# Kernel tuning notes

Measured on AMD Instinct MI355X. Metric: run time of the kernel, lower is better.

Reference implementation:

```python
import jax, jax.numpy as jnp
import numpy as np
from functools import partial

VOCAB = 1000
HID = 512
EPS = 1e-3  # Keras BatchNorm default epsilon


def _conv1d(x, w, stride):
    # x: [B,T,C_in], w: [K,C_in,C_out]
    return jax.lax.conv_general_dilated(x, w, window_strides=(stride,), padding='SAME',
                                        dimension_numbers=('NWC', 'WIO', 'NWC'))


def setup_inputs() -> dict:
    key = jax.random.key(0)
    ks = jax.random.split(key, 8)
    s = lambda *sh: 1.0 / np.sqrt(sh[-2] if len(sh) > 1 else sh[-1])
    return {
        'x': jax.random.normal(ks[0], (32, 1600, 80), jnp.float32),
        'y_true': jax.random.randint(ks[1], (32, 201), 0, VOCAB),
        'bn_gamma': jnp.ones((80,), jnp.float32),
        'bn_beta': jnp.zeros((80,), jnp.float32),
        'conv0_w': jax.random.normal(ks[2], (5, 80, 512), jnp.float32) * 0.05,
        'conv0_b': jnp.zeros((512,), jnp.float32),
        'tcr_w': jax.random.normal(ks[3], (4, 5, 512, 512), jnp.float32) * 0.02,
        'tcr_b': jnp.zeros((4, 512), jnp.float32),
        'gru_kernel': jax.random.normal(ks[4], (VOCAB, 3 * HID), jnp.float32) * 0.03,
        'gru_rec_kernel': jax.random.normal(ks[5], (HID, 3 * HID), jnp.float32) * 0.04,
        'gru_bias': jnp.zeros((2, 3 * HID), jnp.float32),
        'fc_w': jax.random.normal(ks[6], (2 * HID, VOCAB), jnp.float32) * 0.03,
        'fc_b': jnp.zeros((VOCAB,), jnp.float32),
    }


def reference(x, y_true, bn_gamma, bn_beta, conv0_w, conv0_b, tcr_w, tcr_b,
              gru_kernel, gru_rec_kernel, gru_bias, fc_w, fc_b):
    # ---- Encoder ----
    # BatchNorm (training mode: batch statistics over batch & time)
    mean = jnp.mean(x, axis=(0, 1))
    var = jnp.var(x, axis=(0, 1))
    h = (x - mean) * jax.lax.rsqrt(var + EPS) * bn_gamma + bn_beta
    # strided Conv1D + relu -> [B, T=800, 512]
    h = jax.nn.relu(_conv1d(h, conv0_w, 2) + conv0_b)
    # Temporal conv residual blocks: out = relu(conv(x)) + x
    for i in range(tcr_w.shape[0]):
        h = jax.nn.relu(_conv1d(h, tcr_w[i], 1) + tcr_b[i]) + h
    enc = h  # [B, T, D]
    B = enc.shape[0]

    # ---- Decoder (teacher forcing, training branch) ----
    y_oh = jax.nn.one_hot(y_true, VOCAB, dtype=jnp.float32)  # [B, U+1, V]
    inputs = jnp.transpose(y_oh[:, :-1, :], (1, 0, 2))       # [U, B, V]
    bi, br = gru_bias[0], gru_bias[1]

    def step(hstate, y_u):
        # Keras GRUCell (reset_after=True)
        mx = y_u @ gru_kernel + bi
        mh = hstate @ gru_rec_kernel + br
        xz, xr, xh = jnp.split(mx, 3, axis=-1)
        hz, hr, hh = jnp.split(mh, 3, axis=-1)
        z = jax.nn.sigmoid(xz + hz)
        r = jax.nn.sigmoid(xr + hr)
        cand = jnp.tanh(xh + r * hh)
        h_new = z * hstate + (1.0 - z) * cand
        # Dot-product attention over encoder states
        scores = jnp.einsum('bd,btd->bt', h_new, enc)
        alpha = jax.nn.softmax(scores, axis=-1)
        ctx = jnp.einsum('bt,btd->bd', alpha, enc)
        # output projection with softmax activation
        y_pred = jax.nn.softmax(jnp.concatenate([h_new, ctx], axis=1) @ fc_w + fc_b, axis=-1)
        return h_new, y_pred

    h0 = jnp.zeros((B, HID), jnp.float32)
    _, outs = jax.lax.scan(step, h0, inputs)  # [U, B, V]
    return jnp.transpose(outs, (1, 0, 2))     # [B, U, V]
```

## Files before the change

### kernel.cpp

```cpp
#include <hip/hip_runtime.h>
#include <cstdint>

typedef _Float16 f16;
typedef __attribute__((ext_vector_type(2))) _Float16 f16x2;
typedef __attribute__((ext_vector_type(8))) _Float16 f16x8;
typedef __attribute__((ext_vector_type(4))) float f32x4;
typedef __attribute__((ext_vector_type(2))) float f32x2;
typedef __attribute__((ext_vector_type(8))) unsigned short us8;
typedef __attribute__((ext_vector_type(4))) int i32x4;

#define NB   32
#define TIN  1600
#define CIN  80
#define TOUT 800
#define DH   512
#define NV   1000
#define NU   200
#define TXP  1604
#define THP  804
#define EPSB 1e-3f
#define EWG  248

__device__ __forceinline__ void st_sys_f16(f16* p, float v)
{
    f16 h = (f16)v;
    short s; __builtin_memcpy(&s, &h, 2);
    int si = (int)s;
    asm volatile("global_store_short %0, %1, off sc0 sc1"
                 :: "v"(p), "v"(si) : "memory");
}

__device__ __forceinline__ void poll_h16(const f16* base, f16x8 v[16])
{
    while (true) {
        asm volatile(
            "global_load_dwordx4 %0, %16, off sc1\n\t"
            "global_load_dwordx4 %1, %16, off offset:64 sc1\n\t"
            "global_load_dwordx4 %2, %16, off offset:128 sc1\n\t"
            "global_load_dwordx4 %3, %16, off offset:192 sc1\n\t"
            "global_load_dwordx4 %4, %16, off offset:256 sc1\n\t"
            "global_load_dwordx4 %5, %16, off offset:320 sc1\n\t"
            "global_load_dwordx4 %6, %16, off offset:384 sc1\n\t"
            "global_load_dwordx4 %7, %16, off offset:448 sc1\n\t"
            "global_load_dwordx4 %8, %16, off offset:512 sc1\n\t"
            "global_load_dwordx4 %9, %16, off offset:576 sc1\n\t"
            "global_load_dwordx4 %10, %16, off offset:640 sc1\n\t"
            "global_load_dwordx4 %11, %16, off offset:704 sc1\n\t"
            "global_load_dwordx4 %12, %16, off offset:768 sc1\n\t"
            "global_load_dwordx4 %13, %16, off offset:832 sc1\n\t"
            "global_load_dwordx4 %14, %16, off offset:896 sc1\n\t"
            "global_load_dwordx4 %15, %16, off offset:960 sc1\n\t"
            "s_waitcnt vmcnt(0)"
            : "=&v"(v[0]), "=&v"(v[1]), "=&v"(v[2]), "=&v"(v[3]),
              "=&v"(v[4]), "=&v"(v[5]), "=&v"(v[6]), "=&v"(v[7]),
              "=&v"(v[8]), "=&v"(v[9]), "=&v"(v[10]), "=&v"(v[11]),
              "=&v"(v[12]), "=&v"(v[13]), "=&v"(v[14]), "=&v"(v[15])
            : "v"(base)
            : "memory");
        f16x8 s0 = v[0] + v[1],   s1 = v[2] + v[3];
        f16x8 s2 = v[4] + v[5],   s3 = v[6] + v[7];
        f16x8 s4 = v[8] + v[9],   s5 = v[10] + v[11];
        f16x8 s6 = v[12] + v[13], s7 = v[14] + v[15];
        s0 += s1; s2 += s3; s4 += s5; s6 += s7;
        s0 += s2; s4 += s6; s0 += s4;
        float r = (float)s0[0] + (float)s0[1] + (float)s0[2] + (float)s0[3]
                + (float)s0[4] + (float)s0[5] + (float)s0[6] + (float)s0[7];
        if (!__any(r != r)) return;
        __builtin_amdgcn_s_sleep(1);
    }
}

__device__ __forceinline__ float fast_tanh(float x)
{
    return 1.f - 2.f / (__expf(2.f * x) + 1.f);
}

__global__ void init_zero(float* gsum, float* gsumsq,
                          int* lcnt, f16* xpad, f16* hbufA, f16* hbufB,
                          f16* Hc)
{
    int tid = blockIdx.x * 256 + threadIdx.x;
    int stride = gridDim.x * 256;
    if (blockIdx.x == 0) {
        if (threadIdx.x < 80) { gsum[threadIdx.x] = 0.f; gsumsq[threadIdx.x] = 0.f; }
        if (threadIdx.x >= 128 && threadIdx.x < 136) lcnt[threadIdx.x - 128] = 0;
    }
    for (int i = tid; i < NB * 4 * CIN; i += stride) {
        int b = i / (4 * CIN), rr = (i / CIN) % 4, c = i % CIN;
        int row = (rr == 0) ? 0 : (1600 + rr);
        xpad[((long)b * TXP + row) * CIN + c] = (f16)0.f;
    }
    for (int i = tid; i < 2 * NB * 4 * DH; i += stride) {
        int q = i; int buf = q / (NB * 4 * DH); q %= NB * 4 * DH;
        int b = q / (4 * DH); int rr = (q / DH) % 4; int dd = q % DH;
        int row = (rr < 2) ? rr : (800 + rr);
        f16* hb = buf ? hbufB : hbufA;
        hb[((long)b * THP + row) * DH + dd] = (f16)0.f;
    }
    us8 sent;
#pragma unroll
    for (int e = 0; e < 8; e++) sent[e] = 0x7FFFu;
    for (int i = tid; i < 6400 * 64; i += stride)
        *(us8*)&Hc[(long)(i >> 6) * 1024 + (i & 63) * 8] = sent;
}

__global__ void transpose_f32_f16(const float* __restrict__ in, int R, int C,
                                  f16* __restrict__ out, int outRows, int outCols)
{
    __shared__ float t[32][33];
    int c0 = blockIdx.x * 32, r0 = blockIdx.y * 32;
    int x = threadIdx.x & 31, y = threadIdx.x >> 5;
    for (int i = y; i < 32; i += 8) {
        int r = r0 + i, c = c0 + x;
        t[i][x] = (r < R && c < C) ? in[(long)r * C + c] : 0.0f;
    }
    __syncthreads();
    for (int i = y; i < 32; i += 8) {
        int orow = c0 + i, ocol = r0 + x;
        if (orow < outRows && ocol < outCols)
            out[(long)orow * outCols + ocol] = (f16)t[x][i];
    }
}

__global__ void bn_stats(const float* __restrict__ x, float* gsum, float* gsumsq)
{
    __shared__ float ls[240], ls2[240];
    const float* base = x + (long)blockIdx.x * 200 * CIN;
    int tid = threadIdx.x;
    if (tid < 240) {
        int c = tid % 80, rg = tid / 80;
        float s = 0.f, s2 = 0.f;
        for (int r = rg; r < 200; r += 3) {
            float v = base[r * CIN + c];
            s += v; s2 += v * v;
        }
        ls[tid] = s; ls2[tid] = s2;
    }
    __syncthreads();
    if (tid < 80) {
        atomicAdd(&gsum[tid],   ls[tid] + ls[tid + 80] + ls[tid + 160]);
        atomicAdd(&gsumsq[tid], ls2[tid] + ls2[tid + 80] + ls2[tid + 160]);
    }
}

__global__ void bn_apply(const float* __restrict__ x, const float* __restrict__ gsum,
                         const float* __restrict__ gsumsq, const float* __restrict__ gamma,
                         const float* __restrict__ beta, f16* __restrict__ xpad)
{
    long idx = (long)blockIdx.x * 256 + threadIdx.x;
    if (idx >= (long)NB * TIN * CIN) return;
    int c = (int)(idx % CIN);
    long bt = idx / CIN;
    int t = (int)(bt % TIN); int b = (int)(bt / TIN);
    float mean = gsum[c] * (1.f / 51200.f);
    float var  = gsumsq[c] * (1.f / 51200.f) - mean * mean;
    float sc = gamma[c] * rsqrtf(var + EPSB);
    float sh = beta[c] - mean * sc;
    xpad[((long)b * TXP + t + 1) * CIN + c] = (f16)(x[idx] * sc + sh);
}

template<int MODE>
__launch_bounds__(256)
__global__ void gemm16(const f16* __restrict__ Ab, long strideA, long slabA,
                       const f16* __restrict__ Bb, long strideB, long slabB,
                       int M, int N, int Kchunks,
                       const float* __restrict__ bias,
                       float* __restrict__ outF)
{
    __shared__ f16 As[64][72];
    __shared__ f16 Bs[128][72];
    const int b = blockIdx.z;
    const f16* Abase = Ab + (long)b * slabA;
    const f16* Bbase = Bb + (long)b * slabB;
    const int m0 = blockIdx.x * 64, n0 = blockIdx.y * 128;
    const int tid = threadIdx.x;
    const int lane = tid & 63, wv = tid >> 6;
    const int lm = lane & 15, lk = lane >> 4;

    f32x4 vzero = {0.f, 0.f, 0.f, 0.f};
    f32x4 acc[4][2];
#pragma unroll
    for (int i = 0; i < 4; i++) { acc[i][0] = vzero; acc[i][1] = vzero; }

    const int srow = tid >> 3, scol = (tid & 7) * 8;

    for (int kc = 0; kc < Kchunks; kc++) {
        int kb = kc * 64;
#pragma unroll
        for (int p = 0; p < 2; p++) {
            int r = srow + p * 32;
            int m = m0 + r; if (m > M - 1) m = M - 1;
            *(us8*)&As[r][scol] = *(const us8*)(Abase + (long)m * strideA + kb + scol);
        }
#pragma unroll
        for (int p = 0; p < 4; p++) {
            int r = srow + p * 32;
            int n = n0 + r; if (n > N - 1) n = N - 1;
            *(us8*)&Bs[r][scol] = *(const us8*)(Bbase + (long)n * strideB + kb + scol);
        }
        __syncthreads();
#pragma unroll
        for (int ks = 0; ks < 2; ks++) {
            f16x8 af[4], bf[2];
#pragma unroll
            for (int mt = 0; mt < 4; mt++)
                af[mt] = *(const f16x8*)&As[mt * 16 + lm][ks * 32 + lk * 8];
#pragma unroll
            for (int nt = 0; nt < 2; nt++)
                bf[nt] = *(const f16x8*)&Bs[wv * 32 + nt * 16 + lm][ks * 32 + lk * 8];
#pragma unroll
            for (int mt = 0; mt < 4; mt++)
#pragma unroll
                for (int nt = 0; nt < 2; nt++)
                    acc[mt][nt] = __builtin_amdgcn_mfma_f32_16x16x32_f16(af[mt], bf[nt], acc[mt][nt], 0, 0, 0);
        }
        __syncthreads();
    }
#pragma unroll
    for (int mt = 0; mt < 4; mt++) {
#pragma unroll
        for (int nt = 0; nt < 2; nt++) {
            int n = n0 + wv * 32 + nt * 16 + lm;
#pragma unroll
            for (int reg = 0; reg < 4; reg++) {
                int m = m0 + mt * 16 + lk * 4 + reg;
                if (m >= M || n >= N) continue;
                float v = acc[mt][nt][reg];
                if (MODE == 2) {
                    outF[((long)b * NU + m) * 800 + n] = v;
                } else {
                    v += bias[n];
                    int u = m >> 5, bb = m & 31;
                    outF[((long)bb * NU + u) * 1000 + n] = v;
                }
            }
        }
    }
}

__device__ void enc_layer(int eb, int tid,
                          const f16* __restrict__ Ab, long strideA, long slabA,
                          const f16* __restrict__ Bb, long strideB,
                          int Kchunks, const float* __restrict__ bias,
                          const f16* __restrict__ resid, f16* __restrict__ outH,
                          long slabRO, f16 As[][72], f16 Bs[][72])
{
    const int lane = tid & 63, wv = tid >> 6;
    const int lm = lane & 15, lk = lane >> 4;
    const int srow = tid >> 3, scol = (tid & 7) * 8;
    f32x4 vzero = {0.f, 0.f, 0.f, 0.f};

    for (int t = eb; t < 1664; t += EWG) {
        int b = t / 52, rem = t - b * 52;
        int m0 = (rem >> 2) * 64, n0 = (rem & 3) * 128;
        const f16* Abase = Ab + (long)b * slabA;

        f32x4 acc[4][2];
#pragma unroll
        for (int i = 0; i < 4; i++) { acc[i][0] = vzero; acc[i][1] = vzero; }

        for (int kc = 0; kc < Kchunks; kc++) {
            int kb = kc * 64;
#pragma unroll
            for (int p = 0; p < 2; p++) {
                int r = srow + p * 32;
                int m = m0 + r; if (m > 799) m = 799;
                *(us8*)&As[r][scol] = *(const us8*)(Abase + (long)m * strideA + kb + scol);
            }
#pragma unroll
            for (int p = 0; p < 4; p++) {
                int r = srow + p * 32;
                *(us8*)&Bs[r][scol] = *(const us8*)(Bb + (long)(n0 + r) * strideB + kb + scol);
            }
            __syncthreads();
#pragma unroll
            for (int ks = 0; ks < 2; ks++) {
                f16x8 af[4], bf[2];
#pragma unroll
                for (int mt = 0; mt < 4; mt++)
                    af[mt] = *(const f16x8*)&As[mt * 16 + lm][ks * 32 + lk * 8];
#pragma unroll
                for (int nt = 0; nt < 2; nt++)
                    bf[nt] = *(const f16x8*)&Bs[wv * 32 + nt * 16 + lm][ks * 32 + lk * 8];
#pragma unroll
                for (int mt = 0; mt < 4; mt++)
#pragma unroll
                    for (int nt = 0; nt < 2; nt++)
                        acc[mt][nt] = __builtin_amdgcn_mfma_f32_16x16x32_f16(af[mt], bf[nt], acc[mt][nt], 0, 0, 0);
            }
            __syncthreads();
        }
#pragma unroll
        for (int mt = 0; mt < 4; mt++) {
#pragma unroll
            for (int nt = 0; nt < 2; nt++) {
                int n = n0 + wv * 32 + nt * 16 + lm;
#pragma unroll
                for (int reg = 0; reg < 4; reg++) {
                    int m = m0 + mt * 16 + lk * 4 + reg;
                    if (m >= 800) continue;
                    float v = acc[mt][nt][reg] + bias[n];
                    v = v > 0.f ? v : 0.f;
                    if (resid) v += (float)resid[(long)b * slabRO + (long)(2 + m) * DH + n];
                    outH[(long)b * slabRO + (long)(2 + m) * DH + n] = (f16)v;
                }
            }
        }
    }
}

__launch_bounds__(256, 1)
__global__ void enc_gru(const f16* __restrict__ wrecT, const float* __restrict__ gk,
                        const float* __restrict__ gbias, const int* __restrict__ ytrue,
                        f16* __restrict__ Hc,
                        const f16* __restrict__ xpad, const f16* __restrict__ w0T,
                        const float* __restrict__ b0, const f16* __restrict__ tcrT,
                        const float* __restrict__ tcrb,
                        f16* __restrict__ hbufA, f16* __restrict__ hbufB,
                        int* __restrict__ lcnt)
{
    const int tid = threadIdx.x;

    if (blockIdx.x < 8) {
        __shared__ int yl[NU * 32];
        const int lane = tid & 63, wv = tid >> 6;
        const int gw = (int)blockIdx.x * 4 + wv;
        const int lm = lane & 15, lk = lane >> 4;
        const int j = gw * 16 + lm;

        for (int i = tid; i < NU * 32; i += 256) {
            int b = i / NU, u = i - b * NU;
            yl[u * 32 + b] = ytrue[b * 201 + u];
        }

        f16x8 wf[3][16];
#pragma unroll
        for (int g = 0; g < 3; g++)
#pragma unroll
            for (int ks = 0; ks < 16; ks++) {
                wf[g][ks] = *(const f16x8*)&wrecT[(long)(g * 512 + j) * 512 + ks * 32 + lk * 8];
                asm volatile("" : "+v"(wf[g][ks]));
            }

        const float biz = gbias[j],        bir = gbias[512 + j],        bic = gbias[1024 + j];
        const float brz = gbias[1536 + j], brr = gbias[1536 + 512 + j], brc = gbias[1536 + 1024 + j];
        f32x4 vzero = {0.f, 0.f, 0.f, 0.f};

        __syncthreads();

        float hold[8];
        float nxz[8], nxr[8], nxh[8], mxz[8], mxr[8], mxh[8];
#pragma unroll
        for (int s = 0; s < 8; s++) {
            hold[s] = 0.f;
            int b = ((s >> 2) << 4) + lk * 4 + (s & 3);
            const float* gkr = gk + (long)yl[b] * 1536;
            nxz[s] = gkr[j]; nxr[s] = gkr[512 + j]; nxh[s] = gkr[1024 + j];
        }

        for (int u = 0; u < NU; u++) {
            int up = (u < NU - 1) ? u + 1 : u;
#pragma unroll
            for (int s = 0; s < 8; s++) {
                int b = ((s >> 2) << 4) + lk * 4 + (s & 3);
                const float* gkr = gk + (long)yl[up * 32 + b] * 1536;
                mxz[s] = gkr[j]; mxr[s] = gkr[512 + j]; mxh[s] = gkr[1024 + j];
            }

            f32x4 acc[3][2];
#pragma unroll
            for (int g = 0; g < 3; g++) { acc[g][0] = vzero; acc[g][1] = vzero; }

            if (u > 0) {
                const f16* baseA = Hc + ((long)(u - 1) * 32 + lm) * 1024 + lk * 8;
                {
                    f16x8 va[16];
                    poll_h16(baseA, va);
#pragma unroll
                    for (int ks = 0; ks < 16; ks++)
#pragma unroll
                        for (int g = 0; g < 3; g++)
                            acc[g][0] = __builtin_amdgcn_mfma_f32_16x16x32_f16(va[ks], wf[g][ks], acc[g][0], 0, 0, 0);
                }
                {
                    f16x8 vb[16];
                    poll_h16(baseA + 16 * 1024, vb);
#pragma unroll
                    for (int ks = 0; ks < 16; ks++)
#pragma unroll
                        for (int g = 0; g < 3; g++)
                            acc[g][1] = __builtin_amdgcn_mfma_f32_16x16x32_f16(vb[ks], wf[g][ks], acc[g][1], 0, 0, 0);
                }
            }

#pragma unroll
            for (int mt = 0; mt < 2; mt++) {
#pragma unroll
                for (int reg = 0; reg < 4; reg++) {
                    int s = mt * 4 + reg;
                    int b = mt * 16 + lk * 4 + reg;
                    float hz = acc[0][mt][reg] + brz;
                    float hr = acc[1][mt][reg] + brr;
                    float hh = acc[2][mt][reg] + brc;
                    float z = 1.f / (1.f + __expf(-(nxz[s] + biz + hz)));
                    float r = 1.f / (1.f + __expf(-(nxr[s] + bir + hr)));
                    float cd = fast_tanh(nxh[s] + bic + r * hh);
                    float hnew = z * hold[s] + (1.f - z) * cd;
                    hold[s] = hnew;
                    st_sys_f16(&Hc[((long)u * 32 + b) * 1024 + j], hnew);
                }
            }
#pragma unroll
            for (int s = 0; s < 8; s++) { nxz[s] = mxz[s]; nxr[s] = mxr[s]; nxh[s] = mxh[s]; }
        }
        asm volatile("s_waitcnt vmcnt(0)" ::: "memory");
        return;
    }

    __shared__ f16 As[64][72];
    __shared__ f16 Bs[128][72];
    const int eb = (int)blockIdx.x - 8;

    enc_layer(eb, tid, xpad, 160, (long)TXP * CIN, w0T, 448, 7, b0,
              nullptr, hbufA, (long)THP * DH, As, Bs);

    const f16* tin = hbufA; f16* tout = hbufB;
    for (int L = 0; L < 4; L++) {
        __syncthreads();
        if (tid == 0) {
            __hip_atomic_fetch_add(&lcnt[L], 1, __ATOMIC_RELEASE, __HIP_MEMORY_SCOPE_AGENT);
            while (__hip_atomic_load(&lcnt[L], __ATOMIC_RELAXED, __HIP_MEMORY_SCOPE_AGENT) < EWG)
                __builtin_amdgcn_s_sleep(8);
            (void)__hip_atomic_load(&lcnt[L], __ATOMIC_ACQUIRE, __HIP_MEMORY_SCOPE_AGENT);
        }
        __syncthreads();

        enc_layer(eb, tid, tin, 512, (long)THP * DH, tcrT + (size_t)L * 512 * 2560, 2560,
                  40, tcrb + L * 512, tin, tout, (long)THP * DH, As, Bs);
        const f16* t2 = tout; tout = (f16*)tin; tin = t2;
    }
}

__global__ void row_softmax(float* __restrict__ base, int len)
{
    float* s = base + (long)blockIdx.x * len;
    int tid = threadIdx.x;
    float v[4]; float mx = -1e30f;
#pragma unroll
    for (int i = 0; i < 4; i++) {
        int idx = tid + i * 256;
        v[i] = (idx < len) ? s[idx] : -1e30f;
        mx = fmaxf(mx, v[i]);
    }
#pragma unroll
    for (int off = 32; off; off >>= 1) mx = fmaxf(mx, __shfl_xor(mx, off));
    __shared__ float red[4], red2[4];
    if ((tid & 63) == 0) red[tid >> 6] = mx;
    __syncthreads();
    mx = fmaxf(fmaxf(red[0], red[1]), fmaxf(red[2], red[3]));
    float sum = 0.f;
#pragma unroll
    for (int i = 0; i < 4; i++) { v[i] = __expf(v[i] - mx); sum += v[i]; }
#pragma unroll
    for (int off = 32; off; off >>= 1) sum += __shfl_xor(sum, off);
    if ((tid & 63) == 0) red2[tid >> 6] = sum;
    __syncthreads();
    sum = red2[0] + red2[1] + red2[2] + red2[3];
    float inv = 1.f / sum;
#pragma unroll
    for (int i = 0; i < 4; i++) {
        int idx = tid + i * 256;
        if (idx < len) s[idx] = v[i] * inv;
    }
}

__global__ void ctx_kernel(const float* __restrict__ scores, const f16* __restrict__ enc,
                           f16* __restrict__ Hc)
{
    __shared__ float al[800][18];
    __shared__ float red[4], red2[4];
    int b = blockIdx.x, ut = blockIdx.y;
    int u0 = ut * 16;
    int tid = threadIdx.x;
    for (int ul = 0; ul < 16; ul++) {
        int u = u0 + ul;
        if (u < NU) {
            const float* arow = scores + ((long)b * NU + u) * 800;
            float v[4]; float mx = -1e30f;
#pragma unroll
            for (int i = 0; i < 4; i++) {
                int idx = tid + i * 256;
                v[i] = (idx < 800) ? arow[idx] : -1e30f;
                mx = fmaxf(mx, v[i]);
            }
#pragma unroll
            for (int off = 32; off; off >>= 1) mx = fmaxf(mx, __shfl_xor(mx, off));
            if ((tid & 63) == 0) red[tid >> 6] = mx;
            __syncthreads();
            mx = fmaxf(fmaxf(red[0], red[1]), fmaxf(red[2], red[3]));
            float sum = 0.f;
#pragma unroll
            for (int i = 0; i < 4; i++) { v[i] = __expf(v[i] - mx); sum += v[i]; }
#pragma unroll
            for (int off = 32; off; off >>= 1) sum += __shfl_xor(sum, off);
            if ((tid & 63) == 0) red2[tid >> 6] = sum;
            __syncthreads();
            sum = red2[0] + red2[1] + red2[2] + red2[3];
            float inv = 1.f / sum;
#pragma unroll
            for (int i = 0; i < 4; i++) {
                int idx = tid + i * 256;
                if (idx < 800) al[idx][ul] = v[i] * inv;
            }
            __syncthreads();
        } else {
            for (int t = tid; t < 800; t += 256) al[t][ul] = 0.f;
        }
    }
    __syncthreads();
    int d0 = tid * 2;
    float a0[16], a1[16];
#pragma unroll
    for (int i = 0; i < 16; i++) { a0[i] = 0.f; a1[i] = 0.f; }
    const f16* encb = enc + ((long)b * THP + 2) * DH + d0;
    for (int t = 0; t < 800; t++) {
        f16x2 e = *(const f16x2*)&encb[(long)t * DH];
        float f0 = (float)e.x, f1 = (float)e.y;
#pragma unroll
        for (int g = 0; g < 8; g++) {
            f32x2 ap = *(const f32x2*)&al[t][2 * g];
            a0[2 * g]     += ap.x * f0; a0[2 * g + 1] += ap.y * f0;
            a1[2 * g]     += ap.x * f1; a1[2 * g + 1] += ap.y * f1;
        }
    }
#pragma unroll
    for (int ul = 0; ul < 16; ul++) {
        int u = u0 + ul;
        if (u < NU) {
            Hc[((long)u * 32 + b) * 1024 + 512 + d0]     = (f16)a0[ul];
            Hc[((long)u * 32 + b) * 1024 + 512 + d0 + 1] = (f16)a1[ul];
        }
    }
}

extern "C" void kernel_launch(void* const* d_in, const int* in_sizes, int n_in,
                              void* d_out, int out_size, void* d_ws, size_t ws_size,
                              hipStream_t stream)
{
    const float* x     = (const float*)d_in[0];
    const int*   ytrue = (const int*)d_in[1];
    const float* gamma = (const float*)d_in[2];
    const float* beta  = (const float*)d_in[3];
    const float* w0    = (const float*)d_in[4];
    const float* b0    = (const float*)d_in[5];
    const float* tcrw  = (const float*)d_in[6];
    const float* tcrb  = (const float*)d_in[7];
    const float* gk    = (const float*)d_in[8];
    const float* grk   = (const float*)d_in[9];
    const float* gbias = (const float*)d_in[10];
    const float* fcw   = (const float*)d_in[11];
    const float* fcb   = (const float*)d_in[12];
    float* out = (float*)d_out;
    (void)in_sizes; (void)n_in; (void)out_size; (void)ws_size;

    char* ws = (char*)d_ws;
    size_t o = 0;
    auto alloc = [&](size_t bytes) { size_t r = o; o += (bytes + 255) & ~(size_t)255; return r; };
    f16*   xpad   = (f16*)(ws + alloc((size_t)NB * TXP * CIN * 2));
    f16*   hbufA  = (f16*)(ws + alloc((size_t)NB * THP * DH * 2));
    f16*   hbufB  = (f16*)(ws + alloc((size_t)NB * THP * DH * 2));
    f16*   Hc     = (f16*)(ws + alloc((size_t)NU * NB * 1024 * 2));
    float* scores = (float*)(ws + alloc((size_t)NB * NU * 800 * 4));
    f16*   w0T    = (f16*)(ws + alloc((size_t)512 * 448 * 2));
    f16*   tcrT   = (f16*)(ws + alloc((size_t)4 * 512 * 2560 * 2));
    f16*   wrecT  = (f16*)(ws + alloc((size_t)1536 * 512 * 2));
    f16*   fcT    = (f16*)(ws + alloc((size_t)1024 * 1024 * 2));
    float* gsum   = (float*)(ws + alloc(80 * 4));
    float* gsumsq = (float*)(ws + alloc(80 * 4));
    int*   lcnt   = (int*)(ws + alloc(64));

    init_zero<<<64, 256, 0, stream>>>(gsum, gsumsq, lcnt, xpad, hbufA, hbufB, Hc);
    transpose_f32_f16<<<dim3(16, 14), 256, 0, stream>>>(w0, 400, 512, w0T, 512, 448);
    for (int i = 0; i < 4; i++)
        transpose_f32_f16<<<dim3(16, 80), 256, 0, stream>>>(tcrw + (size_t)i * 2560 * 512, 2560, 512,
                                                            tcrT + (size_t)i * 512 * 2560, 512, 2560);
    transpose_f32_f16<<<dim3(48, 16), 256, 0, stream>>>(grk, 512, 1536, wrecT, 1536, 512);
    transpose_f32_f16<<<dim3(32, 32), 256, 0, stream>>>(fcw, 1024, 1000, fcT, 1024, 1024);

    bn_stats<<<256, 256, 0, stream>>>(x, gsum, gsumsq);
    bn_apply<<<16000, 256, 0, stream>>>(x, gsum, gsumsq, gamma, beta, xpad);

    enc_gru<<<8 + EWG, 256, 0, stream>>>(wrecT, gk, gbias, ytrue, Hc,
                                         xpad, w0T, b0, tcrT, tcrb, hbufA, hbufB, lcnt);
    const f16* enc = hbufA;

    gemm16<2><<<dim3(4, 7, 32), 256, 0, stream>>>(Hc, 32 * 1024, 1024, enc + 2 * DH, 512, (long)THP * DH,
        200, 800, 8, nullptr, scores);
    ctx_kernel<<<dim3(32, 13), 256, 0, stream>>>(scores, enc, Hc);

    gemm16<3><<<dim3(100, 8, 1), 256, 0, stream>>>(Hc, 1024, 0, fcT, 1024, 0,
        6400, 1000, 16, fcb, out);
    row_softmax<<<6400, 256, 0, stream>>>(out, 1000);
}
```

Measured before the change: 1.653 ms.

## Fuse attention score GEMM into context kernel using MFMA into shared memory

Removes the separate score GEMM launch and its fp32 scores buffer. Each attention block now computes its own 16x800 score tile with 16x16x32 f16 MFMAs, writes it straight into shared memory, then runs the softmax and context accumulation as before. This saves a global round-trip of the scores and one launch. In exchange, the score work is spread across only 416 blocks, and the same Hc buffer is both read (the h half) and written (the ctx half) in one kernel.

```diff
diff --git a/kernel.cpp b/kernel.cpp
--- a/kernel.cpp
+++ b/kernel.cpp
@@ -474,23 +474,50 @@
     }
 }
 
-__global__ void ctx_kernel(const float* __restrict__ scores, const f16* __restrict__ enc,
-                           f16* __restrict__ Hc)
+__launch_bounds__(256)
+__global__ void attn_kernel(const f16* __restrict__ HcIn, const f16* __restrict__ enc,
+                            f16* __restrict__ Hc)
 {
     __shared__ float al[800][18];
     __shared__ float red[4], red2[4];
-    int b = blockIdx.x, ut = blockIdx.y;
-    int u0 = ut * 16;
-    int tid = threadIdx.x;
+    const int b = blockIdx.x, ut = blockIdx.y;
+    const int u0 = ut * 16;
+    const int tid = threadIdx.x;
+    const int lane = tid & 63, wv = tid >> 6;
+    const int lm = lane & 15, lk = lane >> 4;
+
+    int ua = u0 + lm; if (ua > NU - 1) ua = NU - 1;
+    const f16* arow = HcIn + ((long)ua * 32 + b) * 1024 + lk * 8;
+    f16x8 af[16];
+#pragma unroll
+    for (int kc = 0; kc < 16; kc++)
+        af[kc] = *(const f16x8*)(arow + kc * 32);
+
+    const f16* encb = enc + ((long)b * THP + 2) * DH;
+    f32x4 vzero = {0.f, 0.f, 0.f, 0.f};
+    for (int nt = wv; nt < 50; nt += 4) {
+        const f16* brow = encb + (long)(nt * 16 + lm) * DH + lk * 8;
+        f32x4 acc = vzero;
+#pragma unroll
+        for (int kc = 0; kc < 16; kc++) {
+            f16x8 bf = *(const f16x8*)(brow + kc * 32);
+            acc = __builtin_amdgcn_mfma_f32_16x16x32_f16(af[kc], bf, acc, 0, 0, 0);
+        }
+        const int t = nt * 16 + lm;
+#pragma unroll
+        for (int reg = 0; reg < 4; reg++)
+            al[t][lk * 4 + reg] = acc[reg];
+    }
+    __syncthreads();
+
     for (int ul = 0; ul < 16; ul++) {
         int u = u0 + ul;
         if (u < NU) {
-            const float* arow = scores + ((long)b * NU + u) * 800;
             float v[4]; float mx = -1e30f;
 #pragma unroll
             for (int i = 0; i < 4; i++) {
                 int idx = tid + i * 256;
-                v[i] = (idx < 800) ? arow[idx] : -1e30f;
+                v[i] = (idx < 800) ? al[idx][ul] : -1e30f;
                 mx = fmaxf(mx, v[i]);
             }
 #pragma unroll
@@ -518,13 +545,14 @@
         }
     }
     __syncthreads();
+
     int d0 = tid * 2;
     float a0[16], a1[16];
 #pragma unroll
     for (int i = 0; i < 16; i++) { a0[i] = 0.f; a1[i] = 0.f; }
-    const f16* encb = enc + ((long)b * THP + 2) * DH + d0;
+    const f16* encd = enc + ((long)b * THP + 2) * DH + d0;
     for (int t = 0; t < 800; t++) {
-        f16x2 e = *(const f16x2*)&encb[(long)t * DH];
+        f16x2 e = *(const f16x2*)&encd[(long)t * DH];
         float f0 = (float)e.x, f1 = (float)e.y;
 #pragma unroll
         for (int g = 0; g < 8; g++) {
@@ -570,7 +598,6 @@
     f16*   hbufA  = (f16*)(ws + alloc((size_t)NB * THP * DH * 2));
     f16*   hbufB  = (f16*)(ws + alloc((size_t)NB * THP * DH * 2));
     f16*   Hc     = (f16*)(ws + alloc((size_t)NU * NB * 1024 * 2));
-    float* scores = (float*)(ws + alloc((size_t)NB * NU * 800 * 4));
     f16*   w0T    = (f16*)(ws + alloc((size_t)512 * 448 * 2));
     f16*   tcrT   = (f16*)(ws + alloc((size_t)4 * 512 * 2560 * 2));
     f16*   wrecT  = (f16*)(ws + alloc((size_t)1536 * 512 * 2));
@@ -594,9 +621,7 @@
                                          xpad, w0T, b0, tcrT, tcrb, hbufA, hbufB, lcnt);
     const f16* enc = hbufA;
 
-    gemm16<2><<<dim3(4, 7, 32), 256, 0, stream>>>(Hc, 32 * 1024, 1024, enc + 2 * DH, 512, (long)THP * DH,
-        200, 800, 8, nullptr, scores);
-    ctx_kernel<<<dim3(32, 13), 256, 0, stream>>>(scores, enc, Hc);
+    attn_kernel<<<dim3(32, 13), 256, 0, stream>>>(Hc, enc, Hc);
 
     gemm16<3><<<dim3(100, 8, 1), 256, 0, stream>>>(Hc, 1024, 0, fcT, 1024, 0,
         6400, 1000, 16, fcb, out);
```

After: 1.671 ms. No clear change (+1.1%).

## Co-locate GRU recurrence blocks on one XCD and poll via shared L2

Applied to the files above, without the earlier changes.

Blocks read their XCC_ID and take roles dynamically after a grid-wide arrival barrier. The eight GRU recurrence blocks are all placed on a single XCD, so the per-step hidden-state exchange can use L2-coherent stores and loads (sc0) instead of system-scope sc1 traffic. If an sc0 poll keeps missing, it falls back to sc1 polling. The risks are the extra startup barrier, the assumption that some XCD hosts at least eight blocks, and reliance on undocumented coherence behaviour.

```diff
diff --git a/kernel.cpp b/kernel.cpp
--- a/kernel.cpp
+++ b/kernel.cpp
@@ -21,51 +21,100 @@
 #define EPSB 1e-3f
 #define EWG  248
 
-__device__ __forceinline__ void st_sys_f16(f16* p, float v)
+__device__ __forceinline__ void st_l2_f16(f16* p, float v)
 {
     f16 h = (f16)v;
     short s; __builtin_memcpy(&s, &h, 2);
     int si = (int)s;
-    asm volatile("global_store_short %0, %1, off sc0 sc1"
+    asm volatile("global_store_short %0, %1, off sc0"
                  :: "v"(p), "v"(si) : "memory");
 }
 
-__device__ __forceinline__ void poll_h16(const f16* base, f16x8 v[16])
-{
+__device__ __forceinline__ void load16_sc0(const f16* base, f16x8 v[16])
+{
+    asm volatile(
+        "global_load_dwordx4 %0, %16, off sc0\n\t"
+        "global_load_dwordx4 %1, %16, off offset:64 sc0\n\t"
+        "global_load_dwordx4 %2, %16, off offset:128 sc0\n\t"
+        "global_load_dwordx4 %3, %16, off offset:192 sc0\n\t"
+        "global_load_dwordx4 %4, %16, off offset:256 sc0\n\t"
+        "global_load_dwordx4 %5, %16, off offset:320 sc0\n\t"
+        "global_load_dwordx4 %6, %16, off offset:384 sc0\n\t"
+        "global_load_dwordx4 %7, %16, off offset:448 sc0\n\t"
+        "global_load_dwordx4 %8, %16, off offset:512 sc0\n\t"
+        "global_load_dwordx4 %9, %16, off offset:576 sc0\n\t"
+        "global_load_dwordx4 %10, %16, off offset:640 sc0\n\t"
+        "global_load_dwordx4 %11, %16, off offset:704 sc0\n\t"
+        "global_load_dwordx4 %12, %16, off offset:768 sc0\n\t"
+        "global_load_dwordx4 %13, %16, off offset:832 sc0\n\t"
+        "global_load_dwordx4 %14, %16, off offset:896 sc0\n\t"
+        "global_load_dwordx4 %15, %16, off offset:960 sc0\n\t"
+        "s_waitcnt vmcnt(0)"
+        : "=&v"(v[0]), "=&v"(v[1]), "=&v"(v[2]), "=&v"(v[3]),
+          "=&v"(v[4]), "=&v"(v[5]), "=&v"(v[6]), "=&v"(v[7]),
+          "=&v"(v[8]), "=&v"(v[9]), "=&v"(v[10]), "=&v"(v[11]),
+          "=&v"(v[12]), "=&v"(v[13]), "=&v"(v[14]), "=&v"(v[15])
+        : "v"(base)
+        : "memory");
+}
+__device__ __forceinline__ void load16_sc1(const f16* base, f16x8 v[16])
+{
+    asm volatile(
+        "global_load_dwordx4 %0, %16, off sc1\n\t"
+        "global_load_dwordx4 %1, %16, off offset:64 sc1\n\t"
+        "global_load_dwordx4 %2, %16, off offset:128 sc1\n\t"
+        "global_load_dwordx4 %3, %16, off offset:192 sc1\n\t"
+        "global_load_dwordx4 %4, %16, off offset:256 sc1\n\t"
+        "global_load_dwordx4 %5, %16, off offset:320 sc1\n\t"
+        "global_load_dwordx4 %6, %16, off offset:384 sc1\n\t"
+        "global_load_dwordx4 %7, %16, off offset:448 sc1\n\t"
+        "global_load_dwordx4 %8, %16, off offset:512 sc1\n\t"
+        "global_load_dwordx4 %9, %16, off offset:576 sc1\n\t"
+        "global_load_dwordx4 %10, %16, off offset:640 sc1\n\t"
+        "global_load_dwordx4 %11, %16, off offset:704 sc1\n\t"
+        "global_load_dwordx4 %12, %16, off offset:768 sc1\n\t"
+        "global_load_dwordx4 %13, %16, off offset:832 sc1\n\t"
+        "global_load_dwordx4 %14, %16, off offset:896 sc1\n\t"
+        "global_load_dwordx4 %15, %16, off offset:960 sc1\n\t"
+        "s_waitcnt vmcnt(0)"
+        : "=&v"(v[0]), "=&v"(v[1]), "=&v"(v[2]), "=&v"(v[3]),
+          "=&v"(v[4]), "=&v"(v[5]), "=&v"(v[6]), "=&v"(v[7]),
+          "=&v"(v[8]), "=&v"(v[9]), "=&v"(v[10]), "=&v"(v[11]),
+          "=&v"(v[12]), "=&v"(v[13]), "=&v"(v[14]), "=&v"(v[15])
+        : "v"(base)
+        : "memory");
+}
+
+__device__ __forceinline__ bool h16_ok(const f16x8 v[16])
+{
+    f16x8 s0 = v[0] + v[1],   s1 = v[2] + v[3];
+    f16x8 s2 = v[4] + v[5],   s3 = v[6] + v[7];
+    f16x8 s4 = v[8] + v[9],   s5 = v[10] + v[11];
+    f16x8 s6 = v[12] + v[13], s7 = v[14] + v[15];
+    s0 += s1; s2 += s3; s4 += s5; s6 += s7;
+    s0 += s2; s4 += s6; s0 += s4;
+    float r = (float)s0[0] + (float)s0[1] + (float)s0[2] + (float)s0[3]
+            + (float)s0[4] + (float)s0[5] + (float)s0[6] + (float)s0[7];
+    return !__any(r != r);
+}
+
+__device__ __forceinline__ void poll_l2(const f16* base, f16x8 v[16], int& mode)
+{
+    if (mode == 0) {
+        while (true) {
+            for (int i = 0; i < 64; i++) {
+                load16_sc0(base, v);
+                if (h16_ok(v)) return;
+                __builtin_amdgcn_s_sleep(1);
+            }
+            load16_sc1(base, v);
+            if (h16_ok(v)) { mode = 1; return; }
+            __builtin_amdgcn_s_sleep(1);
+        }
+    }
     while (true) {
-        asm volatile(
-            "global_load_dwordx4 %0, %16, off sc1\n\t"
-            "global_load_dwordx4 %1, %16, off offset:64 sc1\n\t"
-            "global_load_dwordx4 %2, %16, off offset:128 sc1\n\t"
-            "global_load_dwordx4 %3, %16, off offset:192 sc1\n\t"
-            "global_load_dwordx4 %4, %16, off offset:256 sc1\n\t"
-            "global_load_dwordx4 %5, %16, off offset:320 sc1\n\t"
-            "global_load_dwordx4 %6, %16, off offset:384 sc1\n\t"
-            "global_load_dwordx4 %7, %16, off offset:448 sc1\n\t"
-            "global_load_dwordx4 %8, %16, off offset:512 sc1\n\t"
-            "global_load_dwordx4 %9, %16, off offset:576 sc1\n\t"
-            "global_load_dwordx4 %10, %16, off offset:640 sc1\n\t"
-            "global_load_dwordx4 %11, %16, off offset:704 sc1\n\t"
-            "global_load_dwordx4 %12, %16, off offset:768 sc1\n\t"
-            "global_load_dwordx4 %13, %16, off offset:832 sc1\n\t"
-            "global_load_dwordx4 %14, %16, off offset:896 sc1\n\t"
-            "global_load_dwordx4 %15, %16, off offset:960 sc1\n\t"
-            "s_waitcnt vmcnt(0)"
-            : "=&v"(v[0]), "=&v"(v[1]), "=&v"(v[2]), "=&v"(v[3]),
-              "=&v"(v[4]), "=&v"(v[5]), "=&v"(v[6]), "=&v"(v[7]),
-              "=&v"(v[8]), "=&v"(v[9]), "=&v"(v[10]), "=&v"(v[11]),
-              "=&v"(v[12]), "=&v"(v[13]), "=&v"(v[14]), "=&v"(v[15])
-            : "v"(base)
-            : "memory");
-        f16x8 s0 = v[0] + v[1],   s1 = v[2] + v[3];
-        f16x8 s2 = v[4] + v[5],   s3 = v[6] + v[7];
-        f16x8 s4 = v[8] + v[9],   s5 = v[10] + v[11];
-        f16x8 s6 = v[12] + v[13], s7 = v[14] + v[15];
-        s0 += s1; s2 += s3; s4 += s5; s6 += s7;
-        s0 += s2; s4 += s6; s0 += s4;
-        float r = (float)s0[0] + (float)s0[1] + (float)s0[2] + (float)s0[3]
-                + (float)s0[4] + (float)s0[5] + (float)s0[6] + (float)s0[7];
-        if (!__any(r != r)) return;
+        load16_sc1(base, v);
+        if (h16_ok(v)) return;
         __builtin_amdgcn_s_sleep(1);
     }
 }
@@ -83,7 +132,7 @@
     int stride = gridDim.x * 256;
     if (blockIdx.x == 0) {
         if (threadIdx.x < 80) { gsum[threadIdx.x] = 0.f; gsumsq[threadIdx.x] = 0.f; }
-        if (threadIdx.x >= 128 && threadIdx.x < 136) lcnt[threadIdx.x - 128] = 0;
+        if (threadIdx.x >= 128 && threadIdx.x < 144) lcnt[threadIdx.x - 128] = 0;
     }
     for (int i = tid; i < NB * 4 * CIN; i += stride) {
         int b = i / (4 * CIN), rr = (i / CIN) % 4, c = i % CIN;
@@ -321,10 +370,31 @@
 {
     const int tid = threadIdx.x;
 
-    if (blockIdx.x < 8) {
+    __shared__ int sRole, sWid;
+    if (tid == 0) {
+        unsigned int xcd;
+        asm volatile("s_getreg_b32 %0, hwreg(HW_REG_XCC_ID)" : "=s"(xcd));
+        xcd &= 7;
+        int slot = __hip_atomic_fetch_add(&lcnt[8 + xcd], 1, __ATOMIC_RELAXED, __HIP_MEMORY_SCOPE_AGENT);
+        __hip_atomic_fetch_add(&lcnt[5], 1, __ATOMIC_RELEASE, __HIP_MEMORY_SCOPE_AGENT);
+        while (__hip_atomic_load(&lcnt[5], __ATOMIC_RELAXED, __HIP_MEMORY_SCOPE_AGENT) < 8 + EWG)
+            __builtin_amdgcn_s_sleep(2);
+        (void)__hip_atomic_load(&lcnt[5], __ATOMIC_ACQUIRE, __HIP_MEMORY_SCOPE_AGENT);
+        int target = 0;
+        for (int x = 0; x < 8; x++) {
+            int c = __hip_atomic_load(&lcnt[8 + x], __ATOMIC_RELAXED, __HIP_MEMORY_SCOPE_AGENT);
+            if (c >= 8) { target = x; break; }
+        }
+        if ((int)xcd == target && slot < 8) { sRole = slot; sWid = 0; }
+        else { sRole = -1; sWid = __hip_atomic_fetch_add(&lcnt[6], 1, __ATOMIC_RELAXED, __HIP_MEMORY_SCOPE_AGENT); }
+    }
+    __syncthreads();
+    const int role = sRole, wid = sWid;
+
+    if (role >= 0) {
         __shared__ int yl[NU * 32];
         const int lane = tid & 63, wv = tid >> 6;
-        const int gw = (int)blockIdx.x * 4 + wv;
+        const int gw = role * 4 + wv;
         const int lm = lane & 15, lk = lane >> 4;
         const int j = gw * 16 + lm;
 
@@ -358,6 +428,7 @@
             nxz[s] = gkr[j]; nxr[s] = gkr[512 + j]; nxh[s] = gkr[1024 + j];
         }
 
+        int mode = 0;
         for (int u = 0; u < NU; u++) {
             int up = (u < NU - 1) ? u + 1 : u;
 #pragma unroll
@@ -375,7 +446,7 @@
                 const f16* baseA = Hc + ((long)(u - 1) * 32 + lm) * 1024 + lk * 8;
                 {
                     f16x8 va[16];
-                    poll_h16(baseA, va);
+                    poll_l2(baseA, va, mode);
 #pragma unroll
                     for (int ks = 0; ks < 16; ks++)
 #pragma unroll
@@ -384,7 +455,7 @@
                 }
                 {
                     f16x8 vb[16];
-                    poll_h16(baseA + 16 * 1024, vb);
+                    poll_l2(baseA + 16 * 1024, vb, mode);
 #pragma unroll
                     for (int ks = 0; ks < 16; ks++)
 #pragma unroll
@@ -407,7 +478,7 @@
                     float cd = fast_tanh(nxh[s] + bic + r * hh);
                     float hnew = z * hold[s] + (1.f - z) * cd;
                     hold[s] = hnew;
-                    st_sys_f16(&Hc[((long)u * 32 + b) * 1024 + j], hnew);
+                    st_l2_f16(&Hc[((long)u * 32 + b) * 1024 + j], hnew);
                 }
             }
 #pragma unroll
@@ -419,7 +490,7 @@
 
     __shared__ f16 As[64][72];
     __shared__ f16 Bs[128][72];
-    const int eb = (int)blockIdx.x - 8;
+    const int eb = wid;
 
     enc_layer(eb, tid, xpad, 160, (long)TXP * CIN, w0T, 448, 7, b0,
               nullptr, hbufA, (long)THP * DH, As, Bs);
```

Measured after the change: 1.729 ms. 4.6% more time.
